# Optimization experiments

Measured on AMD Instinct MI355X. Metric: run time of the kernel, lower is better.

## Reference

```python
import jax, jax.numpy as jnp
import numpy as np

B, S, D, H = 4, 2048, 512, 8
DH = D // H  # 64


def setup_inputs() -> dict:
    key = jax.random.key(0)
    ks = jax.random.split(key, 7)
    scale = 1.0 / np.sqrt(D)
    return {
        "in_query": jax.random.normal(ks[0], (B, S, D), dtype=jnp.float32),
        "in_key": jax.random.normal(ks[1], (B, S, D), dtype=jnp.float32),
        "in_value": jax.random.normal(ks[2], (B, S, D), dtype=jnp.float32),
        "W_q": jax.random.normal(ks[3], (D, D), dtype=jnp.float32) * scale,
        "W_k": jax.random.normal(ks[4], (D, D), dtype=jnp.float32) * scale,
        "W_v": jax.random.normal(ks[5], (D, D), dtype=jnp.float32) * scale,
        "W_out": jax.random.normal(ks[6], (D, D), dtype=jnp.float32) * scale,
    }


def _split_heads(x):
    # [B, S, D] -> [B, H, S, DH]
    return x.reshape(B, S, H, DH).transpose(0, 2, 1, 3)


def reference(in_query, in_key, in_value, W_q, W_k, W_v, W_out):
    q = _split_heads(in_query @ W_q)   # [B,H,S,DH]
    k = _split_heads(in_key @ W_k)
    v = _split_heads(in_value @ W_v)
    scores = jnp.einsum("bhqd,bhkd->bhqk", q, k) / jnp.sqrt(jnp.float32(DH))
    attn = jax.nn.softmax(scores, axis=-1)  # dropout p=0 -> identity
    out = jnp.einsum("bhqk,bhkd->bhqd", attn, v)  # [B,H,S,DH]
    out = out.transpose(0, 2, 1, 3).reshape(B, S, D)
    return out @ W_out
```

## Files before the change

kernel.cpp:

```cpp
#include <hip/hip_runtime.h>
#include <hip/hip_bf16.h>
#include <cstdint>
#include <cstddef>


typedef __bf16 bf16;
typedef __attribute__((ext_vector_type(8))) __bf16 bf16x8;
typedef __attribute__((ext_vector_type(4))) __bf16 bf16x4;
typedef __attribute__((ext_vector_type(4))) float floatx4;

#define MFMA16(a, b, c) __builtin_amdgcn_mfma_f32_16x16x32_bf16(a, b, c, 0, 0, 0)

#define GLD16(gp, lp)                                              \
  __builtin_amdgcn_global_load_lds(                                \
      (const __attribute__((address_space(1))) unsigned int*)(gp), \
      (__attribute__((address_space(3))) unsigned int*)(lp), 16, 0, 0)

#define PIPE_TOP()                                     \
  do {                                                 \
    asm volatile("s_waitcnt vmcnt(0)" ::: "memory");   \
    __builtin_amdgcn_s_barrier();                      \
    __builtin_amdgcn_sched_barrier(0);                 \
  } while (0)

#define LGKM_BARRIER()                                 \
  do {                                                 \
    asm volatile("s_waitcnt lgkmcnt(0)" ::: "memory"); \
    __builtin_amdgcn_sched_barrier(0);                 \
    __builtin_amdgcn_s_barrier();                      \
    __builtin_amdgcn_sched_barrier(0);                 \
  } while (0)

__device__ __forceinline__ void split2(float x, bf16& hi, bf16& lo) {
  hi = (bf16)x;
  lo = (bf16)(x - (float)hi);
}

__global__ __launch_bounds__(256) void k_split_w(
    const float* __restrict__ Wq, const float* __restrict__ Wk,
    const float* __restrict__ Wv, const float* __restrict__ Wo,
    bf16* __restrict__ wt_hi, bf16* __restrict__ wt_lo) {
  __shared__ float tile[64][65];
  const int w = blockIdx.z;
  const float* W = (w == 0) ? Wq : (w == 1) ? Wk : (w == 2) ? Wv : Wo;
  const int kb = blockIdx.y * 64, nb = blockIdx.x * 64;
  const int tid = threadIdx.x;
  const int col = tid & 63, rbase = tid >> 6;
#pragma unroll
  for (int i = 0; i < 16; i++) {
    int row = rbase + i * 4;
    tile[row][col] = W[(size_t)(kb + row) * 512 + nb + col];
  }
  __syncthreads();
#pragma unroll
  for (int i = 0; i < 16; i++) {
    int nrow = rbase + i * 4;
    float v = tile[col][nrow];
    bf16 hi, lo;
    split2(v, hi, lo);
    size_t o = (size_t)w * 262144 + (size_t)(nb + nrow) * 512 + (kb + col);
    wt_hi[o] = hi;
    wt_lo[o] = lo;
  }
}

__global__ __launch_bounds__(256, 3) void k_proj_qkv(
    const float* __restrict__ Xq, const float* __restrict__ Xk,
    const float* __restrict__ Xv,
    const bf16* __restrict__ wt_hi, const bf16* __restrict__ wt_lo,
    bf16* __restrict__ Q_hi, bf16* __restrict__ Q_lo,
    bf16* __restrict__ K, bf16* __restrict__ Vt) {
  const int P = blockIdx.x;
  const int c_all = P >> 5, within = P & 31;
  const int n_idx = within >> 3, i8 = within & 7;
  const int which = c_all >> 3;
  const int g = ((c_all & 7) << 3) | i8;
  const int m0 = g * 128, n0 = n_idx * 128;

  const float* X = (which == 0) ? Xq : (which == 1) ? Xk : Xv;
  const uint8_t* Bhb = (const uint8_t*)(wt_hi + (size_t)which * 262144);
  const uint8_t* Blb = (const uint8_t*)(wt_lo + (size_t)which * 262144);
  const uint8_t* Xb = (const uint8_t*)X;
  const int tid = threadIdx.x, wave = tid >> 6, lane = tid & 63;
  const int l15 = lane & 15, l4 = lane >> 4;
  const int Am0 = (wave & 1) * 64, Bn0 = (wave >> 1) * 64;

  __shared__ float sA[128 * 32];
  __shared__ bf16 sBh[128 * 32], sBl[128 * 32];

  int aoff[4], adst[4];
#pragma unroll
  for (int p = 0; p < 4; p++) {
    int slot = p * 256 + tid;
    int row = slot >> 3, phys = slot & 7, lg = phys ^ (row & 7);
    aoff[p] = (m0 + row) * 2048 + lg * 16;
    adst[p] = slot * 16;
  }
  int boff[2], bdst[2];
#pragma unroll
  for (int p = 0; p < 2; p++) {
    int slot = p * 256 + tid;
    int row = slot >> 2, phys = slot & 3, lg = phys ^ (row & 3);
    boff[p] = (n0 + row) * 1024 + lg * 16;
    bdst[p] = slot * 16;
  }

  floatx4 acc[4][4];
#pragma unroll
  for (int i = 0; i < 4; i++)
#pragma unroll
    for (int j = 0; j < 4; j++) acc[i][j] = {0.f, 0.f, 0.f, 0.f};

#pragma unroll
  for (int p = 0; p < 4; p++) GLD16(Xb + aoff[p], (char*)sA + adst[p]);
#pragma unroll
  for (int p = 0; p < 2; p++) {
    GLD16(Bhb + boff[p], (char*)sBh + bdst[p]);
    GLD16(Blb + boff[p], (char*)sBl + bdst[p]);
  }

  for (int kb = 0; kb < 512; kb += 32) {
    PIPE_TOP();

    floatx4 af0[4], af1[4];
    bf16x8 bhf[4], blf[4];
#pragma unroll
    for (int mt = 0; mt < 4; mt++) {
      int row = Am0 + mt * 16 + l15, r7 = row & 7;
      af0[mt] = *(const floatx4*)((const char*)sA + row * 128 + (((2 * l4) ^ r7) * 16));
      af1[mt] = *(const floatx4*)((const char*)sA + row * 128 + (((2 * l4 + 1) ^ r7) * 16));
    }
#pragma unroll
    for (int nt = 0; nt < 4; nt++) {
      int row = Bn0 + nt * 16 + l15, r3 = row & 3;
      bhf[nt] = *(const bf16x8*)((const char*)sBh + row * 64 + ((l4 ^ r3) * 16));
      blf[nt] = *(const bf16x8*)((const char*)sBl + row * 64 + ((l4 ^ r3) * 16));
    }

    LGKM_BARRIER();

    if (kb + 32 < 512) {
      const int nkb = kb + 32;
#pragma unroll
      for (int p = 0; p < 4; p++)
        GLD16(Xb + aoff[p] + nkb * 4, (char*)sA + adst[p]);
#pragma unroll
      for (int p = 0; p < 2; p++) {
        GLD16(Bhb + boff[p] + nkb * 2, (char*)sBh + bdst[p]);
        GLD16(Blb + boff[p] + nkb * 2, (char*)sBl + bdst[p]);
      }
    }

    bf16x8 ah[4], al[4];
#pragma unroll
    for (int mt = 0; mt < 4; mt++) {
#pragma unroll
      for (int j = 0; j < 4; j++) {
        bf16 h, l;
        split2(af0[mt][j], h, l);
        ah[mt][j] = h; al[mt][j] = l;
        split2(af1[mt][j], h, l);
        ah[mt][4 + j] = h; al[mt][4 + j] = l;
      }
    }
#pragma unroll
    for (int nt = 0; nt < 4; nt++) {
#pragma unroll
      for (int mt = 0; mt < 4; mt++) {
        acc[mt][nt] = MFMA16(ah[mt], bhf[nt], acc[mt][nt]);
        acc[mt][nt] = MFMA16(ah[mt], blf[nt], acc[mt][nt]);
        acc[mt][nt] = MFMA16(al[mt], bhf[nt], acc[mt][nt]);
      }
    }
  }

  const float scale = (which == 0) ? 0.125f : (which == 1) ? 1.44269504f : 1.0f;
#pragma unroll
  for (int mt = 0; mt < 4; mt++) {
#pragma unroll
    for (int nt = 0; nt < 4; nt++) {
      int m_base = m0 + Am0 + mt * 16 + l4 * 4;
      int n = n0 + Bn0 + nt * 16 + l15;
      int h = (n >> 6) & 7, d = n & 63;
      if (which == 2) {
        int kbase = m_base & 2047, b = m_base >> 11;
        int a32 = kbase & ~31, v = (kbase >> 2) & 7;
        int sbase = a32 + 8 * (v & 3) + 4 * (v >> 2);
        bf16x4 pv;
#pragma unroll
        for (int r = 0; r < 4; r++) pv[r] = (bf16)acc[mt][nt][r];
        *(bf16x4*)&Vt[((size_t)(b * 8 + h) * 64 + d) * 2048 + sbase] = pv;
      } else {
#pragma unroll
        for (int r = 0; r < 4; r++) {
          int m = m_base + r;
          int b = m >> 11, s = m & 2047;
          float v = acc[mt][nt][r] * scale;
          size_t o = ((size_t)(b * 8 + h) * 2048 + s) * 64 + d;
          if (which == 0) {
            bf16 hi, lo;
            split2(v, hi, lo);
            Q_hi[o] = hi; Q_lo[o] = lo;
          } else {
            K[o] = (bf16)v;
          }
        }
      }
    }
  }
}

__global__ __launch_bounds__(256, 3) void k_flash(
    const bf16* __restrict__ Q_hi, const bf16* __restrict__ Q_lo,
    const bf16* __restrict__ K, const bf16* __restrict__ Vt,
    bf16* __restrict__ O_hi, bf16* __restrict__ O_lo) {
  const int P = blockIdx.x;
  const int hi4 = P >> 8, rem = P & 255;
  const int qt = rem >> 3;
  const int bh = hi4 * 8 + (rem & 7);
  const int b = bh >> 3, h = bh & 7;
  const int tid = threadIdx.x, wave = tid >> 6, lane = tid & 63;
  const int l15 = lane & 15, l4 = lane >> 4;
  const int q0 = qt * 64;

  __shared__ char smem[50176];
  float* lbuf = (float*)(smem + 49152);

  const uint8_t* Kb = (const uint8_t*)K + (size_t)bh * 2048 * 128;
  const uint8_t* Vb = (const uint8_t*)Vt + (size_t)bh * 64 * 4096;
  int koff[4], voff[4], dst[4];
#pragma unroll
  for (int p = 0; p < 4; p++) {
    int slot = p * 256 + tid;
    {
      int row = slot >> 3, phys = slot & 7, lg = phys ^ (row & 7);
      koff[p] = row * 128 + lg * 16;
    }
    {
      int row = slot >> 4, phys = slot & 15, lg = phys ^ (row & 15);
      voff[p] = row * 4096 + lg * 16;
    }
    dst[p] = slot * 16;
  }

#pragma unroll
  for (int p = 0; p < 4; p++) {
    GLD16(Kb + koff[p], smem + dst[p]);
    GLD16(Vb + voff[p], smem + 16384 + dst[p]);
  }

#pragma unroll
  for (int nt = 0; nt < 4; nt++) {
#pragma unroll
    for (int ks = 0; ks < 2; ks++) {
      const bf16* ph =
          Q_hi + ((size_t)bh * 2048 + q0 + nt * 16 + l15) * 64 + ks * 32 + l4 * 8;
      const bf16* pl =
          Q_lo + ((size_t)bh * 2048 + q0 + nt * 16 + l15) * 64 + ks * 32 + l4 * 8;
      *(bf16x8*)(smem + 32768 + ((nt * 2 + ks) * 64 + lane) * 16) =
          *(const bf16x8*)ph;
      *(bf16x8*)(smem + 40960 + ((nt * 2 + ks) * 64 + lane) * 16) =
          *(const bf16x8*)pl;
    }
  }

  float lp[4] = {0.f, 0.f, 0.f, 0.f};
  floatx4 oacc[4][4];
#pragma unroll
  for (int i = 0; i < 4; i++)
#pragma unroll
    for (int j = 0; j < 4; j++) oacc[i][j] = {0.f, 0.f, 0.f, 0.f};

  __syncthreads();

  for (int j0 = 0; j0 < 2048; j0 += 128) {
    PIPE_TOP();

    const char* sK = smem;
    const char* sV = smem + 16384;

    bf16x8 kf[2][2];
#pragma unroll
    for (int kt = 0; kt < 2; kt++) {
      int row = wave * 32 + kt * 16 + l15, r7 = row & 7;
#pragma unroll
      for (int ks = 0; ks < 2; ks++)
        kf[ks][kt] =
            *(const bf16x8*)(sK + row * 128 + (((ks * 4 + l4) ^ r7) * 16));
    }
    bf16x8 vf[4];
#pragma unroll
    for (int nt = 0; nt < 4; nt++) {
      int row = nt * 16 + l15;
      vf[nt] =
          *(const bf16x8*)(sV + row * 256 + (((wave * 4 + l4) ^ l15) * 16));
    }

    LGKM_BARRIER();

    if (j0 + 128 < 2048) {
      const size_t nj = (size_t)(j0 + 128);
#pragma unroll
      for (int p = 0; p < 4; p++) {
        GLD16(Kb + nj * 128 + koff[p], smem + dst[p]);
        GLD16(Vb + nj * 2 + voff[p], smem + 16384 + dst[p]);
      }
    }

    floatx4 sc[2][4];
#pragma unroll
    for (int kt = 0; kt < 2; kt++)
#pragma unroll
      for (int nt = 0; nt < 4; nt++)
        sc[kt][nt] = {-24.f, -24.f, -24.f, -24.f};
#pragma unroll
    for (int ks = 0; ks < 2; ks++) {
#pragma unroll
      for (int nt = 0; nt < 4; nt++) {
        bf16x8 qhf =
            *(const bf16x8*)(smem + 32768 + ((nt * 2 + ks) * 64 + lane) * 16);
        bf16x8 qlf =
            *(const bf16x8*)(smem + 40960 + ((nt * 2 + ks) * 64 + lane) * 16);
        sc[0][nt] = MFMA16(kf[ks][0], qhf, sc[0][nt]);
        sc[0][nt] = MFMA16(kf[ks][0], qlf, sc[0][nt]);
        sc[1][nt] = MFMA16(kf[ks][1], qhf, sc[1][nt]);
        sc[1][nt] = MFMA16(kf[ks][1], qlf, sc[1][nt]);
      }
    }

    bf16x8 pf[4];
#pragma unroll
    for (int nt = 0; nt < 4; nt++) {
#pragma unroll
      for (int r = 0; r < 4; r++) {
        float p0 = __builtin_amdgcn_exp2f(sc[0][nt][r]);
        float p1 = __builtin_amdgcn_exp2f(sc[1][nt][r]);
        lp[nt] += p0 + p1;
        pf[nt][r] = (bf16)p0;
        pf[nt][4 + r] = (bf16)p1;
      }
    }

#pragma unroll
    for (int nt = 0; nt < 4; nt++) {
#pragma unroll
      for (int mq = 0; mq < 4; mq++)
        oacc[mq][nt] = MFMA16(pf[mq], vf[nt], oacc[mq][nt]);
    }
  }

#pragma unroll
  for (int nt = 0; nt < 4; nt++) {
    lp[nt] += __shfl_xor(lp[nt], 16, 64);
    lp[nt] += __shfl_xor(lp[nt], 32, 64);
  }
  __syncthreads();
  if (l4 == 0) {
#pragma unroll
    for (int nt = 0; nt < 4; nt++) lbuf[wave * 64 + nt * 16 + l15] = lp[nt];
  }
  floatx4* red = (floatx4*)smem;
#pragma unroll
  for (int phase = 0; phase < 2; phase++) {
    if (wave >= 1) {
#pragma unroll
      for (int i = 0; i < 8; i++) {
        int mq = phase * 2 + (i >> 2);
        red[(wave - 1) * 512 + i * 64 + lane] = oacc[mq][i & 3];
      }
    }
    __syncthreads();
    if (wave == 0) {
#pragma unroll
      for (int i = 0; i < 8; i++) {
        int mq = phase * 2 + (i >> 2);
        oacc[mq][i & 3] += red[i * 64 + lane] + red[512 + i * 64 + lane] +
                           red[1024 + i * 64 + lane];
      }
    }
    __syncthreads();
  }
  if (wave == 0) {
    float lt[4];
#pragma unroll
    for (int nt = 0; nt < 4; nt++)
      lt[nt] = lbuf[nt * 16 + l15] + lbuf[64 + nt * 16 + l15] +
               lbuf[128 + nt * 16 + l15] + lbuf[192 + nt * 16 + l15];
    float rl[4][4];
#pragma unroll
    for (int mq = 0; mq < 4; mq++)
#pragma unroll
      for (int r = 0; r < 4; r++)
        rl[mq][r] = 1.0f / __shfl(lt[mq], (lane & 48) | (l4 * 4 + r), 64);
#pragma unroll
    for (int mq = 0; mq < 4; mq++) {
#pragma unroll
      for (int nt = 0; nt < 4; nt++) {
#pragma unroll
        for (int r = 0; r < 4; r++) {
          float v = oacc[mq][nt][r] * rl[mq][r];
          int gs = q0 + mq * 16 + l4 * 4 + r;
          int gd = h * 64 + nt * 16 + l15;
          size_t o = ((size_t)b * 2048 + gs) * 512 + gd;
          bf16 hi, lo;
          split2(v, hi, lo);
          O_hi[o] = hi;
          O_lo[o] = lo;
        }
      }
    }
  }
}

__global__ __launch_bounds__(256, 2) void k_proj_out(
    const bf16* __restrict__ O_hi, const bf16* __restrict__ O_lo,
    const bf16* __restrict__ wt_hi, const bf16* __restrict__ wt_lo,
    float* __restrict__ out) {
  const int P = blockIdx.x;
  const int g = P & 127, n_idx = P >> 7;
  const int m0 = g * 64, n0 = n_idx * 128;

  const uint8_t* Ahb = (const uint8_t*)O_hi;
  const uint8_t* Alb = (const uint8_t*)O_lo;
  const uint8_t* Bhb = (const uint8_t*)(wt_hi + (size_t)3 * 262144);
  const uint8_t* Blb = (const uint8_t*)(wt_lo + (size_t)3 * 262144);
  const int tid = threadIdx.x, wave = tid >> 6, lane = tid & 63;
  const int l15 = lane & 15, l4 = lane >> 4;
  const int Am0 = (wave & 1) * 32, Bn0 = (wave >> 1) * 64;

  __shared__ bf16 sAh[64 * 32], sAl[64 * 32];
  __shared__ bf16 sBh[128 * 32], sBl[128 * 32];

  int aoff, adst;
  {
    int slot = tid;
    int row = slot >> 2, phys = slot & 3, lg = phys ^ (row & 3);
    aoff = (m0 + row) * 1024 + lg * 16;
    adst = slot * 16;
  }
  int boff[2], bdst[2];
#pragma unroll
  for (int p = 0; p < 2; p++) {
    int slot = p * 256 + tid;
    int row = slot >> 2, phys = slot & 3, lg = phys ^ (row & 3);
    boff[p] = (n0 + row) * 1024 + lg * 16;
    bdst[p] = slot * 16;
  }

  floatx4 acc[2][4];
#pragma unroll
  for (int i = 0; i < 2; i++)
#pragma unroll
    for (int j = 0; j < 4; j++) acc[i][j] = {0.f, 0.f, 0.f, 0.f};

  GLD16(Ahb + aoff, (char*)sAh + adst);
  GLD16(Alb + aoff, (char*)sAl + adst);
#pragma unroll
  for (int p = 0; p < 2; p++) {
    GLD16(Bhb + boff[p], (char*)sBh + bdst[p]);
    GLD16(Blb + boff[p], (char*)sBl + bdst[p]);
  }

  for (int kb = 0; kb < 512; kb += 32) {
    PIPE_TOP();

    bf16x8 ah[2], al[2], bhf[4], blf[4];
#pragma unroll
    for (int mt = 0; mt < 2; mt++) {
      int row = Am0 + mt * 16 + l15, r3 = row & 3;
      ah[mt] = *(const bf16x8*)((const char*)sAh + row * 64 + ((l4 ^ r3) * 16));
      al[mt] = *(const bf16x8*)((const char*)sAl + row * 64 + ((l4 ^ r3) * 16));
    }
#pragma unroll
    for (int nt = 0; nt < 4; nt++) {
      int row = Bn0 + nt * 16 + l15, r3 = row & 3;
      bhf[nt] = *(const bf16x8*)((const char*)sBh + row * 64 + ((l4 ^ r3) * 16));
      blf[nt] = *(const bf16x8*)((const char*)sBl + row * 64 + ((l4 ^ r3) * 16));
    }

    LGKM_BARRIER();

    if (kb + 32 < 512) {
      const int nkb = kb + 32;
      GLD16(Ahb + aoff + nkb * 2, (char*)sAh + adst);
      GLD16(Alb + aoff + nkb * 2, (char*)sAl + adst);
#pragma unroll
      for (int p = 0; p < 2; p++) {
        GLD16(Bhb + boff[p] + nkb * 2, (char*)sBh + bdst[p]);
        GLD16(Blb + boff[p] + nkb * 2, (char*)sBl + bdst[p]);
      }
    }

#pragma unroll
    for (int nt = 0; nt < 4; nt++) {
#pragma unroll
      for (int mt = 0; mt < 2; mt++) {
        acc[mt][nt] = MFMA16(ah[mt], bhf[nt], acc[mt][nt]);
        acc[mt][nt] = MFMA16(ah[mt], blf[nt], acc[mt][nt]);
        acc[mt][nt] = MFMA16(al[mt], bhf[nt], acc[mt][nt]);
      }
    }
  }
#pragma unroll
  for (int mt = 0; mt < 2; mt++) {
#pragma unroll
    for (int nt = 0; nt < 4; nt++) {
#pragma unroll
      for (int r = 0; r < 4; r++) {
        int m = m0 + Am0 + mt * 16 + l4 * 4 + r;
        int n = n0 + Bn0 + nt * 16 + l15;
        out[(size_t)m * 512 + n] = acc[mt][nt][r];
      }
    }
  }
}

extern "C" void kernel_launch(void* const* d_in, const int* in_sizes, int n_in,
                              void* d_out, int out_size, void* d_ws, size_t ws_size,
                              hipStream_t stream) {
  (void)in_sizes; (void)n_in; (void)out_size; (void)ws_size;
  const float* Xq = (const float*)d_in[0];
  const float* Xk = (const float*)d_in[1];
  const float* Xv = (const float*)d_in[2];
  const float* Wq = (const float*)d_in[3];
  const float* Wk = (const float*)d_in[4];
  const float* Wv = (const float*)d_in[5];
  const float* Wo = (const float*)d_in[6];
  float* out = (float*)d_out;

  char* ws = (char*)d_ws;
  size_t off = 0;
  auto alloc = [&](size_t n) {
    void* p = ws + off;
    off += (n + 255) & ~(size_t)255;
    return p;
  };
  const size_t NW = 4 * 262144;
  const size_t NE = 4194304;
  bf16* wt_hi = (bf16*)alloc(NW * 2);
  bf16* wt_lo = (bf16*)alloc(NW * 2);
  bf16* Qh = (bf16*)alloc(NE * 2);
  bf16* Ql = (bf16*)alloc(NE * 2);
  bf16* Kk = (bf16*)alloc(NE * 2);
  bf16* Vt = (bf16*)alloc(NE * 2);
  bf16* Oh = (bf16*)alloc(NE * 2);
  bf16* Ol = (bf16*)alloc(NE * 2);

  k_split_w<<<dim3(8, 8, 4), dim3(256), 0, stream>>>(Wq, Wk, Wv, Wo, wt_hi, wt_lo);
  k_proj_qkv<<<dim3(768), dim3(256), 0, stream>>>(Xq, Xk, Xv, wt_hi, wt_lo,
                                                  Qh, Ql, Kk, Vt);
  k_flash<<<dim3(1024), dim3(256), 0, stream>>>(Qh, Ql, Kk, Vt, Oh, Ol);
  k_proj_out<<<dim3(512), dim3(256), 0, stream>>>(Oh, Ol, wt_hi, wt_lo, out);
}
```

Before: 218.6 us.

## Pre-split X to bf16 hi/lo, double-buffer flash K/V, keep Q in registers, add setprio

Result: no change. 217.4 us (-0.6%).

```diff
diff --git a/kernel.cpp b/kernel.cpp
--- a/kernel.cpp
+++ b/kernel.cpp
@@ -64,9 +64,30 @@
   }
 }
 
-__global__ __launch_bounds__(256, 3) void k_proj_qkv(
+__global__ __launch_bounds__(256) void k_split_x(
     const float* __restrict__ Xq, const float* __restrict__ Xk,
     const float* __restrict__ Xv,
+    bf16* __restrict__ Xh, bf16* __restrict__ Xl) {
+  const int total = 3 * 1048576;
+  for (int j = blockIdx.x * blockDim.x + threadIdx.x; j < total;
+       j += gridDim.x * blockDim.x) {
+    int w = j >> 20, off = j & 1048575;
+    const float* X = (w == 0) ? Xq : (w == 1) ? Xk : Xv;
+    floatx4 v = *(const floatx4*)(X + (size_t)off * 4);
+    bf16x4 hv, lv;
+#pragma unroll
+    for (int r = 0; r < 4; r++) {
+      bf16 h, l;
+      split2(v[r], h, l);
+      hv[r] = h; lv[r] = l;
+    }
+    *(bf16x4*)(Xh + (size_t)w * 4194304 + (size_t)off * 4) = hv;
+    *(bf16x4*)(Xl + (size_t)w * 4194304 + (size_t)off * 4) = lv;
+  }
+}
+
+__global__ __launch_bounds__(256, 3) void k_proj_qkv(
+    const bf16* __restrict__ Xh, const bf16* __restrict__ Xl,
     const bf16* __restrict__ wt_hi, const bf16* __restrict__ wt_lo,
     bf16* __restrict__ Q_hi, bf16* __restrict__ Q_lo,
     bf16* __restrict__ K, bf16* __restrict__ Vt) {
@@ -77,32 +98,25 @@
   const int g = ((c_all & 7) << 3) | i8;
   const int m0 = g * 128, n0 = n_idx * 128;
 
-  const float* X = (which == 0) ? Xq : (which == 1) ? Xk : Xv;
+  const uint8_t* Ahb = (const uint8_t*)(Xh + (size_t)which * 4194304);
+  const uint8_t* Alb = (const uint8_t*)(Xl + (size_t)which * 4194304);
   const uint8_t* Bhb = (const uint8_t*)(wt_hi + (size_t)which * 262144);
   const uint8_t* Blb = (const uint8_t*)(wt_lo + (size_t)which * 262144);
-  const uint8_t* Xb = (const uint8_t*)X;
   const int tid = threadIdx.x, wave = tid >> 6, lane = tid & 63;
   const int l15 = lane & 15, l4 = lane >> 4;
   const int Am0 = (wave & 1) * 64, Bn0 = (wave >> 1) * 64;
 
-  __shared__ float sA[128 * 32];
+  __shared__ bf16 sAh[128 * 32], sAl[128 * 32];
   __shared__ bf16 sBh[128 * 32], sBl[128 * 32];
 
-  int aoff[4], adst[4];
-#pragma unroll
-  for (int p = 0; p < 4; p++) {
-    int slot = p * 256 + tid;
-    int row = slot >> 3, phys = slot & 7, lg = phys ^ (row & 7);
-    aoff[p] = (m0 + row) * 2048 + lg * 16;
-    adst[p] = slot * 16;
-  }
-  int boff[2], bdst[2];
+  int aoff[2], boff[2], dstp[2];
 #pragma unroll
   for (int p = 0; p < 2; p++) {
     int slot = p * 256 + tid;
     int row = slot >> 2, phys = slot & 3, lg = phys ^ (row & 3);
+    aoff[p] = (m0 + row) * 1024 + lg * 16;
     boff[p] = (n0 + row) * 1024 + lg * 16;
-    bdst[p] = slot * 16;
+    dstp[p] = slot * 16;
   }
 
   floatx4 acc[4][4];
@@ -112,23 +126,22 @@
     for (int j = 0; j < 4; j++) acc[i][j] = {0.f, 0.f, 0.f, 0.f};
 
 #pragma unroll
-  for (int p = 0; p < 4; p++) GLD16(Xb + aoff[p], (char*)sA + adst[p]);
-#pragma unroll
   for (int p = 0; p < 2; p++) {
-    GLD16(Bhb + boff[p], (char*)sBh + bdst[p]);
-    GLD16(Blb + boff[p], (char*)sBl + bdst[p]);
+    GLD16(Ahb + aoff[p], (char*)sAh + dstp[p]);
+    GLD16(Alb + aoff[p], (char*)sAl + dstp[p]);
+    GLD16(Bhb + boff[p], (char*)sBh + dstp[p]);
+    GLD16(Blb + boff[p], (char*)sBl + dstp[p]);
   }
 
   for (int kb = 0; kb < 512; kb += 32) {
     PIPE_TOP();
 
-    floatx4 af0[4], af1[4];
-    bf16x8 bhf[4], blf[4];
+    bf16x8 ah[4], al[4], bhf[4], blf[4];
 #pragma unroll
     for (int mt = 0; mt < 4; mt++) {
-      int row = Am0 + mt * 16 + l15, r7 = row & 7;
-      af0[mt] = *(const floatx4*)((const char*)sA + row * 128 + (((2 * l4) ^ r7) * 16));
-      af1[mt] = *(const floatx4*)((const char*)sA + row * 128 + (((2 * l4 + 1) ^ r7) * 16));
+      int row = Am0 + mt * 16 + l15, r3 = row & 3;
+      ah[mt] = *(const bf16x8*)((const char*)sAh + row * 64 + ((l4 ^ r3) * 16));
+      al[mt] = *(const bf16x8*)((const char*)sAl + row * 64 + ((l4 ^ r3) * 16));
     }
 #pragma unroll
     for (int nt = 0; nt < 4; nt++) {
@@ -142,27 +155,15 @@
     if (kb + 32 < 512) {
       const int nkb = kb + 32;
 #pragma unroll
-      for (int p = 0; p < 4; p++)
-        GLD16(Xb + aoff[p] + nkb * 4, (char*)sA + adst[p]);
-#pragma unroll
       for (int p = 0; p < 2; p++) {
-        GLD16(Bhb + boff[p] + nkb * 2, (char*)sBh + bdst[p]);
-        GLD16(Blb + boff[p] + nkb * 2, (char*)sBl + bdst[p]);
-      }
-    }
-
-    bf16x8 ah[4], al[4];
-#pragma unroll
-    for (int mt = 0; mt < 4; mt++) {
-#pragma unroll
-      for (int j = 0; j < 4; j++) {
-        bf16 h, l;
-        split2(af0[mt][j], h, l);
-        ah[mt][j] = h; al[mt][j] = l;
-        split2(af1[mt][j], h, l);
-        ah[mt][4 + j] = h; al[mt][4 + j] = l;
-      }
-    }
+        GLD16(Ahb + aoff[p] + nkb * 2, (char*)sAh + dstp[p]);
+        GLD16(Alb + aoff[p] + nkb * 2, (char*)sAl + dstp[p]);
+        GLD16(Bhb + boff[p] + nkb * 2, (char*)sBh + dstp[p]);
+        GLD16(Blb + boff[p] + nkb * 2, (char*)sBl + dstp[p]);
+      }
+    }
+
+    __builtin_amdgcn_s_setprio(1);
 #pragma unroll
     for (int nt = 0; nt < 4; nt++) {
 #pragma unroll
@@ -172,6 +173,7 @@
         acc[mt][nt] = MFMA16(al[mt], bhf[nt], acc[mt][nt]);
       }
     }
+    __builtin_amdgcn_s_setprio(0);
   }
 
   const float scale = (which == 0) ? 0.125f : (which == 1) ? 1.44269504f : 1.0f;
@@ -210,7 +212,7 @@
   }
 }
 
-__global__ __launch_bounds__(256, 3) void k_flash(
+__global__ __launch_bounds__(256, 2) void k_flash(
     const bf16* __restrict__ Q_hi, const bf16* __restrict__ Q_lo,
     const bf16* __restrict__ K, const bf16* __restrict__ Vt,
     bf16* __restrict__ O_hi, bf16* __restrict__ O_lo) {
@@ -223,8 +225,8 @@
   const int l15 = lane & 15, l4 = lane >> 4;
   const int q0 = qt * 64;
 
-  __shared__ char smem[50176];
-  float* lbuf = (float*)(smem + 49152);
+  __shared__ char smem[2 * 32768 + 1024];
+  float* lbuf = (float*)(smem + 65536);
 
   const uint8_t* Kb = (const uint8_t*)K + (size_t)bh * 2048 * 128;
   const uint8_t* Vb = (const uint8_t*)Vt + (size_t)bh * 64 * 4096;
@@ -249,19 +251,15 @@
     GLD16(Vb + voff[p], smem + 16384 + dst[p]);
   }
 
+  bf16x8 qh[4][2], ql[4][2];
 #pragma unroll
   for (int nt = 0; nt < 4; nt++) {
-#pragma unroll
-    for (int ks = 0; ks < 2; ks++) {
-      const bf16* ph =
-          Q_hi + ((size_t)bh * 2048 + q0 + nt * 16 + l15) * 64 + ks * 32 + l4 * 8;
-      const bf16* pl =
-          Q_lo + ((size_t)bh * 2048 + q0 + nt * 16 + l15) * 64 + ks * 32 + l4 * 8;
-      *(bf16x8*)(smem + 32768 + ((nt * 2 + ks) * 64 + lane) * 16) =
-          *(const bf16x8*)ph;
-      *(bf16x8*)(smem + 40960 + ((nt * 2 + ks) * 64 + lane) * 16) =
-          *(const bf16x8*)pl;
-    }
+    const bf16* ph = Q_hi + ((size_t)bh * 2048 + q0 + nt * 16 + l15) * 64 + l4 * 8;
+    const bf16* pl = Q_lo + ((size_t)bh * 2048 + q0 + nt * 16 + l15) * 64 + l4 * 8;
+    qh[nt][0] = *(const bf16x8*)ph;
+    qh[nt][1] = *(const bf16x8*)(ph + 32);
+    ql[nt][0] = *(const bf16x8*)pl;
+    ql[nt][1] = *(const bf16x8*)(pl + 32);
   }
 
   float lp[4] = {0.f, 0.f, 0.f, 0.f};
@@ -271,13 +269,12 @@
 #pragma unroll
     for (int j = 0; j < 4; j++) oacc[i][j] = {0.f, 0.f, 0.f, 0.f};
 
-  __syncthreads();
-
+  int cur = 0;
   for (int j0 = 0; j0 < 2048; j0 += 128) {
     PIPE_TOP();
 
-    const char* sK = smem;
-    const char* sV = smem + 16384;
+    const char* sK = smem + cur * 32768;
+    const char* sV = sK + 16384;
 
     bf16x8 kf[2][2];
 #pragma unroll
@@ -296,14 +293,13 @@
           *(const bf16x8*)(sV + row * 256 + (((wave * 4 + l4) ^ l15) * 16));
     }
 
-    LGKM_BARRIER();
-
     if (j0 + 128 < 2048) {
+      char* nb = smem + (cur ^ 1) * 32768;
       const size_t nj = (size_t)(j0 + 128);
 #pragma unroll
       for (int p = 0; p < 4; p++) {
-        GLD16(Kb + nj * 128 + koff[p], smem + dst[p]);
-        GLD16(Vb + nj * 2 + voff[p], smem + 16384 + dst[p]);
+        GLD16(Kb + nj * 128 + koff[p], nb + dst[p]);
+        GLD16(Vb + nj * 2 + voff[p], nb + 16384 + dst[p]);
       }
     }
 
@@ -313,20 +309,18 @@
 #pragma unroll
       for (int nt = 0; nt < 4; nt++)
         sc[kt][nt] = {-24.f, -24.f, -24.f, -24.f};
+    __builtin_amdgcn_s_setprio(1);
 #pragma unroll
     for (int ks = 0; ks < 2; ks++) {
 #pragma unroll
       for (int nt = 0; nt < 4; nt++) {
-        bf16x8 qhf =
-            *(const bf16x8*)(smem + 32768 + ((nt * 2 + ks) * 64 + lane) * 16);
-        bf16x8 qlf =
-            *(const bf16x8*)(smem + 40960 + ((nt * 2 + ks) * 64 + lane) * 16);
-        sc[0][nt] = MFMA16(kf[ks][0], qhf, sc[0][nt]);
-        sc[0][nt] = MFMA16(kf[ks][0], qlf, sc[0][nt]);
-        sc[1][nt] = MFMA16(kf[ks][1], qhf, sc[1][nt]);
-        sc[1][nt] = MFMA16(kf[ks][1], qlf, sc[1][nt]);
-      }
-    }
+        sc[0][nt] = MFMA16(kf[ks][0], qh[nt][ks], sc[0][nt]);
+        sc[0][nt] = MFMA16(kf[ks][0], ql[nt][ks], sc[0][nt]);
+        sc[1][nt] = MFMA16(kf[ks][1], qh[nt][ks], sc[1][nt]);
+        sc[1][nt] = MFMA16(kf[ks][1], ql[nt][ks], sc[1][nt]);
+      }
+    }
+    __builtin_amdgcn_s_setprio(0);
 
     bf16x8 pf[4];
 #pragma unroll
@@ -341,12 +335,15 @@
       }
     }
 
+    __builtin_amdgcn_s_setprio(1);
 #pragma unroll
     for (int nt = 0; nt < 4; nt++) {
 #pragma unroll
       for (int mq = 0; mq < 4; mq++)
         oacc[mq][nt] = MFMA16(pf[mq], vf[nt], oacc[mq][nt]);
     }
+    __builtin_amdgcn_s_setprio(0);
+    cur ^= 1;
   }
 
 #pragma unroll
@@ -491,6 +488,7 @@
       }
     }
 
+    __builtin_amdgcn_s_setprio(1);
 #pragma unroll
     for (int nt = 0; nt < 4; nt++) {
 #pragma unroll
@@ -500,6 +498,7 @@
         acc[mt][nt] = MFMA16(al[mt], bhf[nt], acc[mt][nt]);
       }
     }
+    __builtin_amdgcn_s_setprio(0);
   }
 #pragma unroll
   for (int mt = 0; mt < 2; mt++) {
@@ -537,17 +536,22 @@
   };
   const size_t NW = 4 * 262144;
   const size_t NE = 4194304;
+  const size_t NX = 3 * 4194304;
   bf16* wt_hi = (bf16*)alloc(NW * 2);
   bf16* wt_lo = (bf16*)alloc(NW * 2);
   bf16* Qh = (bf16*)alloc(NE * 2);
   bf16* Ql = (bf16*)alloc(NE * 2);
   bf16* Kk = (bf16*)alloc(NE * 2);
   bf16* Vt = (bf16*)alloc(NE * 2);
-  bf16* Oh = (bf16*)alloc(NE * 2);
-  bf16* Ol = (bf16*)alloc(NE * 2);
+  char* shared_region = (char*)alloc(2 * NX * 2);
+  bf16* Xh = (bf16*)shared_region;
+  bf16* Xl = Xh + NX;
+  bf16* Oh = (bf16*)shared_region;
+  bf16* Ol = Oh + NE;
 
   k_split_w<<<dim3(8, 8, 4), dim3(256), 0, stream>>>(Wq, Wk, Wv, Wo, wt_hi, wt_lo);
-  k_proj_qkv<<<dim3(768), dim3(256), 0, stream>>>(Xq, Xk, Xv, wt_hi, wt_lo,
+  k_split_x<<<dim3(2048), dim3(256), 0, stream>>>(Xq, Xk, Xv, Xh, Xl);
+  k_proj_qkv<<<dim3(768), dim3(256), 0, stream>>>(Xh, Xl, wt_hi, wt_lo,
                                                   Qh, Ql, Kk, Vt);
   k_flash<<<dim3(1024), dim3(256), 0, stream>>>(Qh, Ql, Kk, Vt, Oh, Ol);
   k_proj_out<<<dim3(512), dim3(256), 0, stream>>>(Oh, Ol, wt_hi, wt_lo, out);
```
